# Optimization experiments

Hardware: AMD Instinct MI355X
Metric: run time of the kernel (lower is better)

## Reference

```python
import jax, jax.numpy as jnp
import numpy as np

NUM_EXPERTS = 8
TOP_K = 2
B, L, H = 4, 4096, 1024


def setup_inputs() -> dict:
    key = jax.random.key(0)
    ks = jax.random.split(key, 5)
    s = 1.0 / np.sqrt(H)
    return {
        "hidden_states": jax.random.normal(ks[0], (B, L, H), dtype=jnp.float32),
        "gate_w": jax.random.normal(ks[1], (H, NUM_EXPERTS), dtype=jnp.float32) * s,
        "w1": jax.random.normal(ks[2], (NUM_EXPERTS, H, 2 * H), dtype=jnp.float32) * s,
        "b1": jnp.zeros((NUM_EXPERTS, 2 * H), dtype=jnp.float32),
        "w2": jax.random.normal(ks[3], (NUM_EXPERTS, 2 * H, H), dtype=jnp.float32) * (1.0 / np.sqrt(2 * H)),
        "b2": jnp.zeros((NUM_EXPERTS, H), dtype=jnp.float32),
    }


def reference(hidden_states, gate_w, w1, b1, w2, b2):
    b, l, h = hidden_states.shape
    flat = hidden_states.reshape(-1, h)                      # [T, H]
    router_logits = flat @ gate_w                            # [T, E]
    probs = jax.nn.softmax(router_logits, axis=-1)
    weights, indices = jax.lax.top_k(probs, TOP_K)           # [T, K]
    weights = weights / jnp.sum(weights, axis=-1, keepdims=True)
    # combine[t, e] = sum_k weights[t, k] * 1{indices[t, k] == e}
    onehot = jax.nn.one_hot(indices, NUM_EXPERTS, dtype=flat.dtype)  # [T, K, E]
    combine = jnp.einsum('tk,tke->te', weights, onehot)      # [T, E]
    out = jnp.zeros_like(flat)
    for e in range(NUM_EXPERTS):  # fixed small expert loop; dense-compute, sparse-combine
        hdn = jax.nn.relu(flat @ w1[e] + b1[e])              # [T, 2H]
        y = hdn @ w2[e] + b2[e]                              # [T, H]
        out = out + combine[:, e:e + 1] * y
    return out.reshape(b, l, h)
```

## Files before the change

### kernel.cpp

```cpp
#include <hip/hip_runtime.h>
#include <hip/hip_bf16.h>
#include <stdint.h>

#define T_TOK 16384
#define HD    1024
#define HD2   2048
#define NE    8
#define ROWS  (2*T_TOK)
#define MAXT  264
#define RTOK  32


typedef __bf16 bf16x8 __attribute__((ext_vector_type(8)));
typedef float f32x4 __attribute__((ext_vector_type(4)));
typedef unsigned short u16x8 __attribute__((ext_vector_type(8)));

#define GLD16(g, l) __builtin_amdgcn_global_load_lds( \
    (const __attribute__((address_space(1))) void*)(g), \
    (__attribute__((address_space(3))) void*)(l), 16, 0, 0)

__device__ inline unsigned short f2bf(float f) {
    unsigned int u = __float_as_uint(f);
    unsigned int r = (u + 0x7fffu + ((u >> 16) & 1u)) >> 16;
    return (unsigned short)r;
}

__device__ inline void tile_locate(const int* __restrict__ meta, int mt,
                                   int* e_out, int* r0_out, int* re_out) {
    int o = 0, tb = 0, se = -1, sr0 = 0, sre = 0;
#pragma unroll
    for (int k = 0; k < NE; k++) {
        int c = meta[k * 32];
        int t = (c + 127) >> 7;
        if (mt >= tb && mt < tb + t) {
            se = k;
            sr0 = o + (mt - tb) * 128;
            int re = o + c;
            sre = (sr0 + 128 < re) ? sr0 + 128 : re;
        }
        o += c; tb += t;
    }
    *e_out = se; *r0_out = sr0; *re_out = sre;
}

__global__ __launch_bounds__(256) void cvt_all(const float* __restrict__ w1,
                                               const float* __restrict__ w2,
                                               unsigned short* __restrict__ W1T,
                                               unsigned short* __restrict__ W2T) {
    __shared__ float t[32][33];
    int z = blockIdx.z;
    const float* w; unsigned short* wt; int K, N, e;
    if (z < 8) { w = w1; wt = W1T; K = HD;  N = HD2; e = z; }
    else       { w = w2; wt = W2T; K = HD2; N = HD;  e = z - 8; }
    int n0 = blockIdx.x * 32, k0 = blockIdx.y * 32;
    if (n0 >= N || k0 >= K) return;
    int r = threadIdx.x >> 3;
    int c4 = (threadIdx.x & 7) * 4;
    const float* src = w + ((size_t)e * K + k0 + r) * N + n0 + c4;
    float4 v = *(const float4*)src;
    t[r][c4] = v.x; t[r][c4+1] = v.y; t[r][c4+2] = v.z; t[r][c4+3] = v.w;
    __syncthreads();
    int cc = threadIdx.x & 7;
    ushort4 o;
    o.x = f2bf(t[cc*4+0][r]); o.y = f2bf(t[cc*4+1][r]);
    o.z = f2bf(t[cc*4+2][r]); o.w = f2bf(t[cc*4+3][r]);
    *(ushort4*)(wt + ((size_t)e * N + n0 + r) * K + k0 + cc*4) = o;
}

__global__ __launch_bounds__(256) void router_k(const float* __restrict__ x,
        const float* __restrict__ gw, int* __restrict__ meta,
        int* __restrict__ tok_e, int* __restrict__ tok_slot, float* __restrict__ tok_w,
        unsigned short* __restrict__ xb) {
    __shared__ float g[NE * HD];
    __shared__ int   le[RTOK * 2];
    __shared__ float lw[RTOK * 2];
    __shared__ int   lslot[RTOK * 2];
    __shared__ int   lcnt[NE];
    __shared__ int   lbase[NE];
    for (int i = threadIdx.x; i < NE * HD; i += 256) {
        int k = i >> 3, e = i & 7;
        g[e * HD + k] = gw[i];
    }
    if (threadIdx.x < NE) lcnt[threadIdx.x] = 0;
    __syncthreads();

    int wave = threadIdx.x >> 6, lane = threadIdx.x & 63;
    int t0 = blockIdx.x * RTOK;
    for (int i = 0; i < RTOK / 4; i++) {
        int tt = wave * (RTOK / 4) + i;
        int t = t0 + tt;
        const float4* xr = (const float4*)(x + (size_t)t * HD);
        float acc[NE];
#pragma unroll
        for (int e = 0; e < NE; e++) acc[e] = 0.f;
#pragma unroll
        for (int j = 0; j < HD / 256; j++) {
            float4 xv = xr[lane + 64 * j];
            ushort4 o4;
            o4.x = f2bf(xv.x); o4.y = f2bf(xv.y);
            o4.z = f2bf(xv.z); o4.w = f2bf(xv.w);
            *(ushort4*)(xb + (size_t)t * HD + (lane + 64 * j) * 4) = o4;
#pragma unroll
            for (int e = 0; e < NE; e++) {
                float4 gv = *(const float4*)&g[e * HD + (lane + 64 * j) * 4];
                acc[e] += xv.x * gv.x + xv.y * gv.y + xv.z * gv.z + xv.w * gv.w;
            }
        }
#pragma unroll
        for (int e = 0; e < NE; e++) {
            float v = acc[e];
#pragma unroll
            for (int off = 32; off > 0; off >>= 1) v += __shfl_down(v, off, 64);
            acc[e] = v;
        }
        if (lane == 0) {
            int e1 = 0; float l1 = acc[0];
#pragma unroll
            for (int e = 1; e < NE; e++) if (acc[e] > l1) { l1 = acc[e]; e1 = e; }
            int e2 = -1; float l2 = -3.0e38f;
#pragma unroll
            for (int e = 0; e < NE; e++) if (e != e1 && acc[e] > l2) { l2 = acc[e]; e2 = e; }
            float w1 = 1.f / (1.f + expf(l2 - l1));
            le[tt * 2] = e1;     le[tt * 2 + 1] = e2;
            lw[tt * 2] = w1;     lw[tt * 2 + 1] = 1.f - w1;
        }
    }
    __syncthreads();
    if (threadIdx.x < RTOK * 2)
        lslot[threadIdx.x] = atomicAdd(&lcnt[le[threadIdx.x]], 1);
    __syncthreads();
    if (threadIdx.x < NE)
        lbase[threadIdx.x] = atomicAdd(&meta[threadIdx.x * 32], lcnt[threadIdx.x]);
    __syncthreads();
    if (threadIdx.x < RTOK * 2) {
        int gi = t0 * 2 + threadIdx.x;
        int e = le[threadIdx.x];
        tok_e[gi]    = e;
        tok_slot[gi] = lbase[e] + lslot[threadIdx.x];
        tok_w[gi]    = lw[threadIdx.x];
    }
}

__global__ __launch_bounds__(256) void scatter_k(const int* __restrict__ meta,
        const int* __restrict__ tok_e, const int* __restrict__ tok_slot,
        const float* __restrict__ tok_w, int* __restrict__ rows_tok,
        float* __restrict__ rows_w) {
    int i = blockIdx.x * 256 + threadIdx.x;
    int e = tok_e[i];
    int off = 0;
#pragma unroll
    for (int k = 0; k < NE; k++) {
        int c = meta[k * 32];
        off += (k < e) ? c : 0;
    }
    int r = off + tok_slot[i];
    rows_tok[r] = i >> 1;
    rows_w[r] = tok_w[i];
}


#define ISSUE(KK, NT_) do { \
    int kk_ = (KK) < (NT_) ? (KK) : (NT_) - 1; \
    int bb_ = ((KK) & 1) * 4096; \
    GLD16(pa0 + kk_ * 32, &As[bb_ + (w * 64) * 8]); \
    GLD16(pa1 + kk_ * 32, &As[bb_ + (256 + w * 64) * 8]); \
    GLD16(pb0 + kk_ * 32, &Bs[bb_ + (w * 64) * 8]); \
    GLD16(pb1 + kk_ * 32, &Bs[bb_ + (256 + w * 64) * 8]); } while (0)
#define SB0()   __builtin_amdgcn_sched_barrier(0)
#define VMW4()  do { asm volatile("s_waitcnt vmcnt(4)" ::: "memory"); SB0(); } while (0)
#define VMW0()  do { asm volatile("s_waitcnt vmcnt(0)" ::: "memory"); SB0(); } while (0)
#define BAR()   do { __builtin_amdgcn_s_barrier(); SB0(); } while (0)
#define PRIO(P) __builtin_amdgcn_s_setprio(P)

#define KSTEP(RB) do { \
    bf16x8 af[4], bfr[4]; \
    _Pragma("unroll") \
    for (int in_ = 0; in_ < 4; in_++) { \
        int row_ = wn * 64 + in_ * 16 + rl; \
        int ph_ = q ^ ((row_ >> 1) & 3); \
        bfr[in_] = *(const bf16x8*)&Bs[(RB) + row_ * 32 + ph_ * 8]; \
    } \
    _Pragma("unroll") \
    for (int im_ = 0; im_ < 4; im_++) { \
        int row_ = wm * 64 + im_ * 16 + rl; \
        int ph_ = q ^ ((row_ >> 1) & 3); \
        af[im_] = *(const bf16x8*)&As[(RB) + row_ * 32 + ph_ * 8]; \
    } \
    _Pragma("unroll") \
    for (int im_ = 0; im_ < 4; im_++) \
    _Pragma("unroll") \
    for (int in_ = 0; in_ < 4; in_++) \
        acc[im_][in_] = __builtin_amdgcn_mfma_f32_16x16x32_bf16( \
            af[im_], bfr[in_], acc[im_][in_], 0, 0, 0); } while (0)

__global__ __launch_bounds__(256, 4) void gemm1_k(
    const unsigned short* __restrict__ Xbf,
    const unsigned short* __restrict__ W1T,
    const float* __restrict__ b1,
    const int* __restrict__ meta,
    const int* __restrict__ rows_tok,
    unsigned short* __restrict__ hdn)
{
    __shared__ unsigned short As[2 * 4096];
    __shared__ unsigned short Bs[2 * 4096];
    int id = blockIdx.x;
    int r_ = id & 7, qq = id >> 3;
    int xx = qq & 15, mt = (qq >> 4) * 8 + r_;
    int e, r0, rend;
    tile_locate(meta, mt, &e, &r0, &rend);
    if (e < 0) return;
    int n0 = xx * 128;

    int tid = threadIdx.x, w = tid >> 6, lane = tid & 63;
    int wm = w & 1, wn = w >> 1;
    int rl = lane & 15, q = lane >> 4;

    const unsigned short *pa0, *pa1, *pb0, *pb1;
    {
        int gg = tid, row = gg >> 2, lc = (gg & 3) ^ ((row >> 1) & 3);
        int grow = r0 + row; grow = grow < ROWS - 1 ? grow : ROWS - 1;
        pa0 = Xbf + (size_t)rows_tok[grow] * HD + lc * 8;
        pb0 = W1T + ((size_t)e * HD2 + n0 + row) * HD + lc * 8;
        gg = 256 + tid; row = gg >> 2; lc = (gg & 3) ^ ((row >> 1) & 3);
        grow = r0 + row; grow = grow < ROWS - 1 ? grow : ROWS - 1;
        pa1 = Xbf + (size_t)rows_tok[grow] * HD + lc * 8;
        pb1 = W1T + ((size_t)e * HD2 + n0 + row) * HD + lc * 8;
    }

    f32x4 acc[4][4];
#pragma unroll
    for (int a = 0; a < 4; a++)
#pragma unroll
    for (int b = 0; b < 4; b++)
        acc[a][b] = (f32x4){0.f, 0.f, 0.f, 0.f};

    ISSUE(0, HD / 32);

#pragma unroll 2
    for (int kt = 0; kt < HD / 32; kt++) {
        ISSUE(kt + 1, HD / 32);
        SB0();
        VMW4();
        BAR();
        PRIO(1);
        KSTEP((kt & 1) * 4096);
        PRIO(0);
        BAR();
    }
    VMW0();
    BAR();

    {
        const float* b1e = b1 + (size_t)e * HD2;
        unsigned short* obuf = wn ? (unsigned short*)Bs : (unsigned short*)As;
#pragma unroll
        for (int in = 0; in < 4; in++) {
            int ci = in * 16 + rl;
            float bias = b1e[n0 + wn * 64 + ci];
#pragma unroll
            for (int im = 0; im < 4; im++) {
                int rowb = wm * 64 + im * 16 + q * 4;
#pragma unroll
                for (int j = 0; j < 4; j++) {
                    int row = rowb + j;
                    float v = acc[im][in][j] + bias;
                    v = v > 0.f ? v : 0.f;
                    int gc = ci >> 3;
                    obuf[row * 64 + (((gc ^ (row & 7)) << 3) | (ci & 7))] = f2bf(v);
                }
            }
        }
    }
    BAR();
#pragma unroll
    for (int it = 0; it < 8; it++) {
        int row = it * 16 + (tid >> 4);
        int gran = tid & 15;
        const unsigned short* ibuf = (gran < 8) ? (const unsigned short*)As
                                                : (const unsigned short*)Bs;
        u16x8 v = *(const u16x8*)&ibuf[row * 64 + (((gran & 7) ^ (row & 7)) << 3)];
        int r = r0 + row;
        if (r < rend)
            *(u16x8*)&hdn[(size_t)r * HD2 + n0 + gran * 8] = v;
    }
}

__global__ __launch_bounds__(256, 4) void gemm2_k(
    const unsigned short* __restrict__ hdn,
    const unsigned short* __restrict__ W2T,
    const float* __restrict__ b2,
    const int* __restrict__ meta,
    const int* __restrict__ rows_tok,
    const float* __restrict__ rows_w,
    float* __restrict__ out)
{
    __shared__ unsigned short As[2 * 4096];
    __shared__ unsigned short Bs[2 * 4096];
    int id = blockIdx.x;
    int r_ = id & 7, qq = id >> 3;
    int xx = qq & 7, mt = (qq >> 3) * 8 + r_;
    int e, r0, rend;
    tile_locate(meta, mt, &e, &r0, &rend);
    if (e < 0) return;
    int n0 = xx * 128;

    int tid = threadIdx.x, w = tid >> 6, lane = tid & 63;
    int wm = w & 1, wn = w >> 1;
    int rl = lane & 15, q = lane >> 4;

    const unsigned short *pa0, *pa1, *pb0, *pb1;
    {
        int gg = tid, row = gg >> 2, lc = (gg & 3) ^ ((row >> 1) & 3);
        int grow = r0 + row; grow = grow < ROWS - 1 ? grow : ROWS - 1;
        pa0 = hdn + (size_t)grow * HD2 + lc * 8;
        pb0 = W2T + ((size_t)e * HD + n0 + row) * HD2 + lc * 8;
        gg = 256 + tid; row = gg >> 2; lc = (gg & 3) ^ ((row >> 1) & 3);
        grow = r0 + row; grow = grow < ROWS - 1 ? grow : ROWS - 1;
        pa1 = hdn + (size_t)grow * HD2 + lc * 8;
        pb1 = W2T + ((size_t)e * HD + n0 + row) * HD2 + lc * 8;
    }

    f32x4 acc[4][4];
#pragma unroll
    for (int a = 0; a < 4; a++)
#pragma unroll
    for (int b = 0; b < 4; b++)
        acc[a][b] = (f32x4){0.f, 0.f, 0.f, 0.f};

    ISSUE(0, HD2 / 32);

#pragma unroll 2
    for (int kt = 0; kt < HD2 / 32; kt++) {
        ISSUE(kt + 1, HD2 / 32);
        SB0();
        VMW4();
        BAR();
        PRIO(1);
        KSTEP((kt & 1) * 4096);
        PRIO(0);
        BAR();
    }
    VMW0();

    const float* b2e = b2 + (size_t)e * HD;
    float bias[4];
#pragma unroll
    for (int in = 0; in < 4; in++)
        bias[in] = b2e[n0 + wn * 64 + in * 16 + rl];
#pragma unroll
    for (int im = 0; im < 4; im++) {
        int rb2 = r0 + wm * 64 + im * 16 + q * 4;
#pragma unroll
        for (int j = 0; j < 4; j++) {
            int r = rb2 + j;
            if (r < rend) {
                int tok = rows_tok[r];
                float wt = rows_w[r];
                float* op = out + (size_t)tok * HD + n0 + wn * 64;
#pragma unroll
                for (int in = 0; in < 4; in++) {
                    float v = (acc[im][in][j] + bias[in]) * wt;
                    atomicAdd(op + in * 16 + rl, v);
                }
            }
        }
    }
}

extern "C" void kernel_launch(void* const* d_in, const int* in_sizes, int n_in,
                              void* d_out, int out_size, void* d_ws, size_t ws_size,
                              hipStream_t stream) {
    const float* x  = (const float*)d_in[0];
    const float* gw = (const float*)d_in[1];
    const float* w1 = (const float*)d_in[2];
    const float* b1 = (const float*)d_in[3];
    const float* w2 = (const float*)d_in[4];
    const float* b2 = (const float*)d_in[5];
    float* out = (float*)d_out;

    uint8_t* ws = (uint8_t*)d_ws;
    unsigned short* Xbf = (unsigned short*)(ws);
    unsigned short* W1T = (unsigned short*)(ws + 33554432ull);
    unsigned short* W2T = (unsigned short*)(ws + 67108864ull);
    unsigned short* HDN = (unsigned short*)(ws + 100663296ull);
    int*   meta     = (int*)(ws + 234881024ull);
    int*   tok_e    = meta + 2048;
    int*   tok_slot = tok_e + ROWS;
    float* tok_w    = (float*)(tok_slot + ROWS);
    int*   rows_tok = (int*)(tok_w + ROWS);
    float* rows_w   = (float*)(rows_tok + ROWS);

    hipMemsetAsync(meta, 0, 1024, stream);
    hipMemsetAsync(d_out, 0, (size_t)out_size * sizeof(float), stream);

    cvt_all<<<dim3(64, 64, 16), 256, 0, stream>>>(w1, w2, W1T, W2T);
    router_k<<<T_TOK / RTOK, 256, 0, stream>>>(x, gw, meta, tok_e, tok_slot, tok_w, Xbf);
    scatter_k<<<ROWS / 256, 256, 0, stream>>>(meta, tok_e, tok_slot, tok_w, rows_tok, rows_w);
    gemm1_k<<<16 * MAXT, 256, 0, stream>>>(Xbf, W1T, b1, meta, rows_tok, HDN);
    gemm2_k<<<8 * MAXT, 256, 0, stream>>>(HDN, W2T, b2, meta, rows_tok, rows_w, out);
}
```

Before: 671.5 us.

## Use 256-row tiles in gemm2 and fuse weight conversion with router

```diff
diff --git a/kernel.cpp b/kernel.cpp
--- a/kernel.cpp
+++ b/kernel.cpp
@@ -8,7 +8,9 @@
 #define NE    8
 #define ROWS  (2*T_TOK)
 #define MAXT  264
+#define MT256 136
 #define RTOK  32
+#define NCVT  65536
 
 
 typedef __bf16 bf16x8 __attribute__((ext_vector_type(8)));
@@ -25,58 +27,62 @@
     return (unsigned short)r;
 }
 
-__device__ inline void tile_locate(const int* __restrict__ meta, int mt,
-                                   int* e_out, int* r0_out, int* re_out) {
+__device__ inline void tile_locate_g(const int* __restrict__ meta, int mt, int gran_log2,
+                                     int* e_out, int* r0_out, int* re_out) {
+    int gran = 1 << gran_log2;
     int o = 0, tb = 0, se = -1, sr0 = 0, sre = 0;
 #pragma unroll
     for (int k = 0; k < NE; k++) {
         int c = meta[k * 32];
-        int t = (c + 127) >> 7;
+        int t = (c + gran - 1) >> gran_log2;
         if (mt >= tb && mt < tb + t) {
             se = k;
-            sr0 = o + (mt - tb) * 128;
+            sr0 = o + (mt - tb) * gran;
             int re = o + c;
-            sre = (sr0 + 128 < re) ? sr0 + 128 : re;
+            sre = (sr0 + gran < re) ? sr0 + gran : re;
         }
         o += c; tb += t;
     }
     *e_out = se; *r0_out = sr0; *re_out = sre;
 }
 
-__global__ __launch_bounds__(256) void cvt_all(const float* __restrict__ w1,
-                                               const float* __restrict__ w2,
-                                               unsigned short* __restrict__ W1T,
-                                               unsigned short* __restrict__ W2T) {
-    __shared__ float t[32][33];
-    int z = blockIdx.z;
-    const float* w; unsigned short* wt; int K, N, e;
-    if (z < 8) { w = w1; wt = W1T; K = HD;  N = HD2; e = z; }
-    else       { w = w2; wt = W2T; K = HD2; N = HD;  e = z - 8; }
-    int n0 = blockIdx.x * 32, k0 = blockIdx.y * 32;
-    if (n0 >= N || k0 >= K) return;
-    int r = threadIdx.x >> 3;
-    int c4 = (threadIdx.x & 7) * 4;
-    const float* src = w + ((size_t)e * K + k0 + r) * N + n0 + c4;
-    float4 v = *(const float4*)src;
-    t[r][c4] = v.x; t[r][c4+1] = v.y; t[r][c4+2] = v.z; t[r][c4+3] = v.w;
-    __syncthreads();
-    int cc = threadIdx.x & 7;
-    ushort4 o;
-    o.x = f2bf(t[cc*4+0][r]); o.y = f2bf(t[cc*4+1][r]);
-    o.z = f2bf(t[cc*4+2][r]); o.w = f2bf(t[cc*4+3][r]);
-    *(ushort4*)(wt + ((size_t)e * N + n0 + r) * K + k0 + cc*4) = o;
-}
-
-__global__ __launch_bounds__(256) void router_k(const float* __restrict__ x,
-        const float* __restrict__ gw, int* __restrict__ meta,
-        int* __restrict__ tok_e, int* __restrict__ tok_slot, float* __restrict__ tok_w,
-        unsigned short* __restrict__ xb) {
-    __shared__ float g[NE * HD];
-    __shared__ int   le[RTOK * 2];
-    __shared__ float lw[RTOK * 2];
-    __shared__ int   lslot[RTOK * 2];
-    __shared__ int   lcnt[NE];
-    __shared__ int   lbase[NE];
+__global__ __launch_bounds__(256) void front_k(
+        const float* __restrict__ w1, const float* __restrict__ w2,
+        unsigned short* __restrict__ W1T, unsigned short* __restrict__ W2T,
+        const float* __restrict__ x, const float* __restrict__ gw,
+        int* __restrict__ meta, int* __restrict__ tok_e, int* __restrict__ tok_slot,
+        float* __restrict__ tok_w, unsigned short* __restrict__ xb) {
+    __shared__ float smem[8400];
+    int id = blockIdx.x;
+    if (id < NCVT) {
+        int z = id & 15, rest = id >> 4;
+        int bx = rest & 63, by = rest >> 6;
+        const float* w; unsigned short* wt; int K, N, e;
+        if (z < 8) { w = w1; wt = W1T; K = HD;  N = HD2; e = z; }
+        else       { w = w2; wt = W2T; K = HD2; N = HD;  e = z - 8; }
+        int n0 = bx * 32, k0 = by * 32;
+        if (n0 >= N || k0 >= K) return;
+        float (*t)[33] = (float(*)[33])smem;
+        int r = threadIdx.x >> 3;
+        int c4 = (threadIdx.x & 7) * 4;
+        const float* src = w + ((size_t)e * K + k0 + r) * N + n0 + c4;
+        float4 v = *(const float4*)src;
+        t[r][c4] = v.x; t[r][c4+1] = v.y; t[r][c4+2] = v.z; t[r][c4+3] = v.w;
+        __syncthreads();
+        int cc = threadIdx.x & 7;
+        ushort4 o;
+        o.x = f2bf(t[cc*4+0][r]); o.y = f2bf(t[cc*4+1][r]);
+        o.z = f2bf(t[cc*4+2][r]); o.w = f2bf(t[cc*4+3][r]);
+        *(ushort4*)(wt + ((size_t)e * N + n0 + r) * K + k0 + cc*4) = o;
+        return;
+    }
+    int bid = id - NCVT;
+    float* g     = smem;
+    int*   le    = (int*)&smem[8192];
+    float* lw    = &smem[8256];
+    int*   lslot = (int*)&smem[8320];
+    int*   lcnt  = (int*)&smem[8384];
+    int*   lbase = (int*)&smem[8392];
     for (int i = threadIdx.x; i < NE * HD; i += 256) {
         int k = i >> 3, e = i & 7;
         g[e * HD + k] = gw[i];
@@ -85,7 +91,7 @@
     __syncthreads();
 
     int wave = threadIdx.x >> 6, lane = threadIdx.x & 63;
-    int t0 = blockIdx.x * RTOK;
+    int t0 = bid * RTOK;
     for (int i = 0; i < RTOK / 4; i++) {
         int tt = wave * (RTOK / 4) + i;
         int t = t0 + tt;
@@ -120,9 +126,9 @@
             int e2 = -1; float l2 = -3.0e38f;
 #pragma unroll
             for (int e = 0; e < NE; e++) if (e != e1 && acc[e] > l2) { l2 = acc[e]; e2 = e; }
-            float w1 = 1.f / (1.f + expf(l2 - l1));
+            float w1v = 1.f / (1.f + expf(l2 - l1));
             le[tt * 2] = e1;     le[tt * 2 + 1] = e2;
-            lw[tt * 2] = w1;     lw[tt * 2 + 1] = 1.f - w1;
+            lw[tt * 2] = w1v;    lw[tt * 2 + 1] = 1.f - w1v;
         }
     }
     __syncthreads();
@@ -158,21 +164,22 @@
     rows_w[r] = tok_w[i];
 }
 
-
-#define ISSUE(KK, NT_) do { \
+#define SB0()   __builtin_amdgcn_sched_barrier(0)
+#define VMW4()  do { asm volatile("s_waitcnt vmcnt(4)" ::: "memory"); SB0(); } while (0)
+#define VMW6()  do { asm volatile("s_waitcnt vmcnt(6)" ::: "memory"); SB0(); } while (0)
+#define VMW0()  do { asm volatile("s_waitcnt vmcnt(0)" ::: "memory"); SB0(); } while (0)
+#define BAR()   do { __builtin_amdgcn_s_barrier(); SB0(); } while (0)
+#define PRIO(P) __builtin_amdgcn_s_setprio(P)
+
+#define ISSUE1(KK, NT_) do { \
     int kk_ = (KK) < (NT_) ? (KK) : (NT_) - 1; \
     int bb_ = ((KK) & 1) * 4096; \
     GLD16(pa0 + kk_ * 32, &As[bb_ + (w * 64) * 8]); \
     GLD16(pa1 + kk_ * 32, &As[bb_ + (256 + w * 64) * 8]); \
     GLD16(pb0 + kk_ * 32, &Bs[bb_ + (w * 64) * 8]); \
     GLD16(pb1 + kk_ * 32, &Bs[bb_ + (256 + w * 64) * 8]); } while (0)
-#define SB0()   __builtin_amdgcn_sched_barrier(0)
-#define VMW4()  do { asm volatile("s_waitcnt vmcnt(4)" ::: "memory"); SB0(); } while (0)
-#define VMW0()  do { asm volatile("s_waitcnt vmcnt(0)" ::: "memory"); SB0(); } while (0)
-#define BAR()   do { __builtin_amdgcn_s_barrier(); SB0(); } while (0)
-#define PRIO(P) __builtin_amdgcn_s_setprio(P)
-
-#define KSTEP(RB) do { \
+
+#define KSTEP1(RB) do { \
     bf16x8 af[4], bfr[4]; \
     _Pragma("unroll") \
     for (int in_ = 0; in_ < 4; in_++) { \
@@ -207,7 +214,7 @@
     int r_ = id & 7, qq = id >> 3;
     int xx = qq & 15, mt = (qq >> 4) * 8 + r_;
     int e, r0, rend;
-    tile_locate(meta, mt, &e, &r0, &rend);
+    tile_locate_g(meta, mt, 7, &e, &r0, &rend);
     if (e < 0) return;
     int n0 = xx * 128;
 
@@ -234,16 +241,16 @@
     for (int b = 0; b < 4; b++)
         acc[a][b] = (f32x4){0.f, 0.f, 0.f, 0.f};
 
-    ISSUE(0, HD / 32);
+    ISSUE1(0, HD / 32);
 
 #pragma unroll 2
     for (int kt = 0; kt < HD / 32; kt++) {
-        ISSUE(kt + 1, HD / 32);
+        ISSUE1(kt + 1, HD / 32);
         SB0();
         VMW4();
         BAR();
         PRIO(1);
-        KSTEP((kt & 1) * 4096);
+        KSTEP1((kt & 1) * 4096);
         PRIO(0);
         BAR();
     }
@@ -285,7 +292,39 @@
     }
 }
 
-__global__ __launch_bounds__(256, 4) void gemm2_k(
+#define ISSUE2(KK, NT_) do { \
+    int kk_ = (KK) < (NT_) ? (KK) : (NT_) - 1; \
+    int ba_ = ((KK) & 1) * 8192; \
+    int bb_ = ((KK) & 1) * 4096; \
+    GLD16(pa[0] + kk_ * 32, &As[ba_ + (w * 64) * 8]); \
+    GLD16(pa[1] + kk_ * 32, &As[ba_ + (256 + w * 64) * 8]); \
+    GLD16(pa[2] + kk_ * 32, &As[ba_ + (512 + w * 64) * 8]); \
+    GLD16(pa[3] + kk_ * 32, &As[ba_ + (768 + w * 64) * 8]); \
+    GLD16(pb[0] + kk_ * 32, &Bs[bb_ + (w * 64) * 8]); \
+    GLD16(pb[1] + kk_ * 32, &Bs[bb_ + (256 + w * 64) * 8]); } while (0)
+
+#define KSTEP2(RA, RB) do { \
+    bf16x8 af[8], bfr[4]; \
+    _Pragma("unroll") \
+    for (int in_ = 0; in_ < 4; in_++) { \
+        int row_ = wn * 64 + in_ * 16 + rl; \
+        int ph_ = q ^ ((row_ >> 1) & 3); \
+        bfr[in_] = *(const bf16x8*)&Bs[(RB) + row_ * 32 + ph_ * 8]; \
+    } \
+    _Pragma("unroll") \
+    for (int im_ = 0; im_ < 8; im_++) { \
+        int row_ = wm * 128 + im_ * 16 + rl; \
+        int ph_ = q ^ ((row_ >> 1) & 3); \
+        af[im_] = *(const bf16x8*)&As[(RA) + row_ * 32 + ph_ * 8]; \
+    } \
+    _Pragma("unroll") \
+    for (int im_ = 0; im_ < 8; im_++) \
+    _Pragma("unroll") \
+    for (int in_ = 0; in_ < 4; in_++) \
+        acc[im_][in_] = __builtin_amdgcn_mfma_f32_16x16x32_bf16( \
+            af[im_], bfr[in_], acc[im_][in_], 0, 0, 0); } while (0)
+
+__global__ __launch_bounds__(256, 2) void gemm2_k(
     const unsigned short* __restrict__ hdn,
     const unsigned short* __restrict__ W2T,
     const float* __restrict__ b2,
@@ -294,13 +333,13 @@
     const float* __restrict__ rows_w,
     float* __restrict__ out)
 {
-    __shared__ unsigned short As[2 * 4096];
+    __shared__ unsigned short As[2 * 8192];
     __shared__ unsigned short Bs[2 * 4096];
     int id = blockIdx.x;
     int r_ = id & 7, qq = id >> 3;
     int xx = qq & 7, mt = (qq >> 3) * 8 + r_;
     int e, r0, rend;
-    tile_locate(meta, mt, &e, &r0, &rend);
+    tile_locate_g(meta, mt, 8, &e, &r0, &rend);
     if (e < 0) return;
     int n0 = xx * 128;
 
@@ -308,35 +347,37 @@
     int wm = w & 1, wn = w >> 1;
     int rl = lane & 15, q = lane >> 4;
 
-    const unsigned short *pa0, *pa1, *pb0, *pb1;
-    {
-        int gg = tid, row = gg >> 2, lc = (gg & 3) ^ ((row >> 1) & 3);
+    const unsigned short* pa[4];
+    const unsigned short* pb[2];
+#pragma unroll
+    for (int c = 0; c < 4; c++) {
+        int gg = c * 256 + tid, row = gg >> 2, lc = (gg & 3) ^ ((row >> 1) & 3);
         int grow = r0 + row; grow = grow < ROWS - 1 ? grow : ROWS - 1;
-        pa0 = hdn + (size_t)grow * HD2 + lc * 8;
-        pb0 = W2T + ((size_t)e * HD + n0 + row) * HD2 + lc * 8;
-        gg = 256 + tid; row = gg >> 2; lc = (gg & 3) ^ ((row >> 1) & 3);
-        grow = r0 + row; grow = grow < ROWS - 1 ? grow : ROWS - 1;
-        pa1 = hdn + (size_t)grow * HD2 + lc * 8;
-        pb1 = W2T + ((size_t)e * HD + n0 + row) * HD2 + lc * 8;
-    }
-
-    f32x4 acc[4][4];
-#pragma unroll
-    for (int a = 0; a < 4; a++)
+        pa[c] = hdn + (size_t)grow * HD2 + lc * 8;
+    }
+#pragma unroll
+    for (int c = 0; c < 2; c++) {
+        int gg = c * 256 + tid, row = gg >> 2, lc = (gg & 3) ^ ((row >> 1) & 3);
+        pb[c] = W2T + ((size_t)e * HD + n0 + row) * HD2 + lc * 8;
+    }
+
+    f32x4 acc[8][4];
+#pragma unroll
+    for (int a = 0; a < 8; a++)
 #pragma unroll
     for (int b = 0; b < 4; b++)
         acc[a][b] = (f32x4){0.f, 0.f, 0.f, 0.f};
 
-    ISSUE(0, HD2 / 32);
+    ISSUE2(0, HD2 / 32);
 
 #pragma unroll 2
     for (int kt = 0; kt < HD2 / 32; kt++) {
-        ISSUE(kt + 1, HD2 / 32);
+        ISSUE2(kt + 1, HD2 / 32);
         SB0();
-        VMW4();
+        VMW6();
         BAR();
         PRIO(1);
-        KSTEP((kt & 1) * 4096);
+        KSTEP2((kt & 1) * 8192, (kt & 1) * 4096);
         PRIO(0);
         BAR();
     }
@@ -348,8 +389,8 @@
     for (int in = 0; in < 4; in++)
         bias[in] = b2e[n0 + wn * 64 + in * 16 + rl];
 #pragma unroll
-    for (int im = 0; im < 4; im++) {
-        int rb2 = r0 + wm * 64 + im * 16 + q * 4;
+    for (int im = 0; im < 8; im++) {
+        int rb2 = r0 + wm * 128 + im * 16 + q * 4;
 #pragma unroll
         for (int j = 0; j < 4; j++) {
             int r = rb2 + j;
@@ -393,9 +434,11 @@
     hipMemsetAsync(meta, 0, 1024, stream);
     hipMemsetAsync(d_out, 0, (size_t)out_size * sizeof(float), stream);
 
-    cvt_all<<<dim3(64, 64, 16), 256, 0, stream>>>(w1, w2, W1T, W2T);
-    router_k<<<T_TOK / RTOK, 256, 0, stream>>>(x, gw, meta, tok_e, tok_slot, tok_w, Xbf);
-    scatter_k<<<ROWS / 256, 256, 0, stream>>>(meta, tok_e, tok_slot, tok_w, rows_tok, rows_w);
+    front_k<<<NCVT + T_TOK / RTOK, 256, 0, stream>>>(w1, w2, W1T, W2T,
+                                                     x, gw, meta, tok_e, tok_slot,
+                                                     tok_w, Xbf);
+    scatter_k<<<ROWS / 256, 256, 0, stream>>>(meta, tok_e, tok_slot, tok_w,
+                                              rows_tok, rows_w);
     gemm1_k<<<16 * MAXT, 256, 0, stream>>>(Xbf, W1T, b1, meta, rows_tok, HDN);
-    gemm2_k<<<8 * MAXT, 256, 0, stream>>>(HDN, W2T, b2, meta, rows_tok, rows_w, out);
-}
+    gemm2_k<<<8 * MT256, 256, 0, stream>>>(HDN, W2T, b2, meta, rows_tok, rows_w, out);
+}
```

Result: slower. 749.8 us (+11.7%).
